# Kernel tuning notes

Hardware: AMD Instinct MI355X
Metric: run time of the kernel (lower is better)

## Reference

```python
import math
import jax, jax.numpy as jnp
import numpy as np

N_DIM = 1024
N_HEADS = 16
HEAD_DIM = N_DIM // N_HEADS
B, S = 8, 1024


def setup_inputs() -> dict:
    key = jax.random.key(0)
    ks = jax.random.split(key, 10)
    s = 1.0 / math.sqrt(N_DIM)
    inp = {
        "x": jax.random.normal(ks[0], (B, S, N_DIM), dtype=jnp.float32),
        "padding_mask": jax.random.randint(ks[1], (B, 1, 1, S), 0, 2).astype(bool),
        "Wq": jax.random.uniform(ks[2], (N_DIM, N_DIM), jnp.float32, -s, s),
        "bq": jax.random.uniform(ks[3], (N_DIM,), jnp.float32, -s, s),
        "Wk": jax.random.uniform(ks[4], (N_DIM, N_DIM), jnp.float32, -s, s),
        "bk": jax.random.uniform(ks[5], (N_DIM,), jnp.float32, -s, s),
        "Wv": jax.random.uniform(ks[6], (N_DIM, N_DIM), jnp.float32, -s, s),
        "bv": jax.random.uniform(ks[7], (N_DIM,), jnp.float32, -s, s),
        "Wo": jax.random.uniform(ks[8], (N_DIM, N_DIM), jnp.float32, -s, s),
        "bo": jax.random.uniform(ks[9], (N_DIM,), jnp.float32, -s, s),
    }
    return inp


def _split_heads(t):
    b, s, _ = t.shape
    return t.reshape(b, s, N_HEADS, HEAD_DIM).transpose(0, 2, 1, 3)  # [B,H,S,D]


def reference(x, padding_mask, Wq, bq, Wk, bk, Wv, bv, Wo, bo):
    # nn.Linear: y = x @ W^T + b
    Q = _split_heads(x @ Wq.T + bq)
    K = _split_heads(x @ Wk.T + bk)
    V = _split_heads(x @ Wv.T + bv)
    scale = 1.0 / math.sqrt(HEAD_DIM)
    scores = jnp.einsum('bhqd,bhkd->bhqk', Q, K) * scale
    scores = jnp.where(padding_mask, -jnp.inf, scores)
    attn = jax.nn.softmax(scores, axis=-1)
    attn = jnp.nan_to_num(attn, nan=0.0)  # fully-masked rows -> 0
    ctx = jnp.einsum('bhqk,bhkd->bhqd', attn, V)
    ctx = ctx.transpose(0, 2, 1, 3).reshape(x.shape[0], x.shape[1], N_DIM)
    return ctx @ Wo.T + bo  # dropout is identity in eval mode
```

## Files before the change

### kernel.cpp

```cpp
#include <hip/hip_runtime.h>
#include <hip/hip_bf16.h>
#include <math.h>

#define B_SZ 8
#define SEQ 1024
#define NDIM 1024
#define NH 16
#define HD 64
#define MROWS (B_SZ * SEQ)
#define SCALE_L2E 0.18033688011112042f
#define NEGB (-1e30f)

typedef __attribute__((ext_vector_type(4))) float f32x4;
typedef __attribute__((ext_vector_type(8))) short s16x8;
typedef __attribute__((ext_vector_type(4))) short s16x4;

#define MFMA16(a, b, c) __builtin_amdgcn_mfma_f32_16x16x32_bf16((a), (b), (c), 0, 0, 0)

__device__ __forceinline__ unsigned short f2bf(float f) {
    union { float f; unsigned int u; } v; v.f = f;
    unsigned int r = v.u + 0x7FFFu + ((v.u >> 16) & 1u);
    return (unsigned short)(r >> 16);
}

__device__ __forceinline__ void llds16(const void* g, void* l) {
    __builtin_amdgcn_global_load_lds(
        (const __attribute__((address_space(1))) void*)g,
        (__attribute__((address_space(3))) void*)l, 16, 0, 0);
}

__global__ void prep_mask(const unsigned char* __restrict__ m, float* __restrict__ bias) {
    __shared__ int fl[3];
    if (threadIdx.x < 3) fl[threadIdx.x] = 0;
    __syncthreads();
    int a = 0, o1 = 0, o23 = 0;
    for (int i = threadIdx.x; i < B_SZ * SEQ; i += 1024) {
        unsigned char v = m[i];
        if (v) { int q = i & 3; if (q == 0) a = 1; else if (q == 1) o1 = 1; else o23 = 1; }
    }
    if (a)   atomicOr(&fl[0], 1);
    if (o1)  atomicOr(&fl[1], 1);
    if (o23) atomicOr(&fl[2], 1);
    __syncthreads();
    int fmt;
    if (fl[0] && !fl[1] && !fl[2])      fmt = 0;
    else if (!fl[0] && !fl[1] && fl[2]) fmt = 2;
    else                                fmt = 1;
    for (int i = threadIdx.x; i < B_SZ * SEQ; i += 1024) {
        int t;
        if (fmt == 0)      t = ((const int*)m)[i];
        else if (fmt == 1) t = m[i];
        else               t = (((const float*)m)[i] != 0.f);
        bias[i] = t ? NEGB : 0.f;
    }
}

__global__ void cvt_x(const float* __restrict__ s, unsigned short* __restrict__ d) {
    const int i = (blockIdx.x * 256 + threadIdx.x) * 4;
    float4 v = *(const float4*)(s + i);
    s16x4 o; o[0] = (short)f2bf(v.x); o[1] = (short)f2bf(v.y);
    o[2] = (short)f2bf(v.z); o[3] = (short)f2bf(v.w);
    *(s16x4*)(d + i) = o;
}

__global__ void cvt_w(const float* __restrict__ q, const float* __restrict__ k,
                      const float* __restrict__ v, const float* __restrict__ o,
                      unsigned short* __restrict__ d) {
    const int i = (blockIdx.x * 256 + threadIdx.x) * 4;
    const int which = i >> 20;
    const float* s = (which == 0) ? q : (which == 1) ? k : (which == 2) ? v : o;
    float4 x = *(const float4*)(s + (i & ((1 << 20) - 1)));
    s16x4 p; p[0] = (short)f2bf(x.x); p[1] = (short)f2bf(x.y);
    p[2] = (short)f2bf(x.z); p[3] = (short)f2bf(x.w);
    *(s16x4*)(d + i) = p;
}

#define GBM 128
#define GBK 32

__global__ __launch_bounds__(256) void gemm_qkv(
    const unsigned short* __restrict__ X, const unsigned short* __restrict__ Wb,
    const float* __restrict__ bq, const float* __restrict__ bk, const float* __restrict__ bv,
    unsigned short* __restrict__ Qo, unsigned short* __restrict__ Ko,
    unsigned short* __restrict__ Vt)
{
    __shared__ __align__(16) short As[GBM * GBK];
    __shared__ __align__(16) short Bs[GBM * GBK];

    const int tid = threadIdx.x, lane = tid & 63, w = tid >> 6;
    const int wm = w >> 1, wn = w & 1;
    const int g = lane >> 4, ql = lane & 15;
    const int which = blockIdx.y >> 3, ny = blockIdx.y & 7;
    const int bm = blockIdx.x * GBM, bn = ny * GBM;
    const unsigned short* W = Wb + (size_t)which * (1 << 20);
    const float* bias = (which == 0) ? bq : (which == 1) ? bk : bv;

    f32x4 acc[4][4] = {};

    for (int k0 = 0; k0 < NDIM; k0 += GBK) {
#pragma unroll
        for (int i = 0; i < 2; ++i) {
            const int s = tid + i * 256;
            const int r = s >> 2, kc = (s & 3) * 8;
            llds16(X + (size_t)(bm + r) * NDIM + k0 + kc, &As[s * 8]);
            llds16(W + (size_t)(bn + r) * NDIM + k0 + kc, &Bs[s * 8]);
        }
        __syncthreads();
        s16x8 af[4], bf[4];
#pragma unroll
        for (int f = 0; f < 4; ++f) {
            af[f] = *(const s16x8*)&As[(wm * 64 + f * 16 + ql) * GBK + g * 8];
            bf[f] = *(const s16x8*)&Bs[(wn * 64 + f * 16 + ql) * GBK + g * 8];
        }
#pragma unroll
        for (int i = 0; i < 4; ++i)
#pragma unroll
            for (int j = 0; j < 4; ++j)
                acc[i][j] = MFMA16(af[i], bf[j], acc[i][j]);
        __syncthreads();
    }

    if (which < 2) {
        unsigned short* O = (which == 0) ? Qo : Ko;
#pragma unroll
        for (int j = 0; j < 4; ++j) {
            const int col = bn + wn * 64 + j * 16 + ql;
            const float bv_ = bias[col];
#pragma unroll
            for (int i = 0; i < 4; ++i) {
                const int row0 = bm + wm * 64 + i * 16 + 4 * g;
#pragma unroll
                for (int r = 0; r < 4; ++r)
                    O[(size_t)(row0 + r) * NDIM + col] = f2bf(acc[i][j][r] + bv_);
            }
        }
    } else {
#pragma unroll
        for (int j = 0; j < 4; ++j) {
            const int col = bn + wn * 64 + j * 16 + ql;
            const float bv_ = bias[col];
            const int h = col >> 6, dd = col & 63;
#pragma unroll
            for (int i = 0; i < 4; ++i) {
                const int row0 = bm + wm * 64 + i * 16 + 4 * g;
                const int b_ = row0 >> 10, s_ = row0 & 1023;
                s16x4 pk;
#pragma unroll
                for (int r = 0; r < 4; ++r) pk[r] = (short)f2bf(acc[i][j][r] + bv_);
                *(s16x4*)&Vt[(((size_t)(b_ * NH + h)) * HD + dd) * SEQ + s_] = pk;
            }
        }
    }
}

__global__ __launch_bounds__(256) void gemm_out(
    const unsigned short* __restrict__ X, const unsigned short* __restrict__ W,
    const float* __restrict__ bias, float* __restrict__ out)
{
    __shared__ __align__(16) short As[GBM * GBK];
    __shared__ __align__(16) short Bs[GBM * GBK];

    const int tid = threadIdx.x, lane = tid & 63, w = tid >> 6;
    const int wm = w >> 1, wn = w & 1;
    const int g = lane >> 4, ql = lane & 15;
    const int bm = blockIdx.x * GBM, bn = blockIdx.y * GBM;

    f32x4 acc[4][4] = {};

    for (int k0 = 0; k0 < NDIM; k0 += GBK) {
#pragma unroll
        for (int i = 0; i < 2; ++i) {
            const int s = tid + i * 256;
            const int r = s >> 2, kc = (s & 3) * 8;
            llds16(X + (size_t)(bm + r) * NDIM + k0 + kc, &As[s * 8]);
            llds16(W + (size_t)(bn + r) * NDIM + k0 + kc, &Bs[s * 8]);
        }
        __syncthreads();
        s16x8 af[4], bf[4];
#pragma unroll
        for (int f = 0; f < 4; ++f) {
            af[f] = *(const s16x8*)&As[(wm * 64 + f * 16 + ql) * GBK + g * 8];
            bf[f] = *(const s16x8*)&Bs[(wn * 64 + f * 16 + ql) * GBK + g * 8];
        }
#pragma unroll
        for (int i = 0; i < 4; ++i)
#pragma unroll
            for (int j = 0; j < 4; ++j)
                acc[i][j] = MFMA16(af[i], bf[j], acc[i][j]);
        __syncthreads();
    }

#pragma unroll
    for (int j = 0; j < 4; ++j) {
        const int col = bn + wn * 64 + j * 16 + ql;
        const float bv_ = bias[col];
#pragma unroll
        for (int i = 0; i < 4; ++i) {
            const int row0 = bm + wm * 64 + i * 16 + 4 * g;
#pragma unroll
            for (int r = 0; r < 4; ++r)
                out[(size_t)(row0 + r) * NDIM + col] = acc[i][j][r] + bv_;
        }
    }
}

__global__ __launch_bounds__(256) void attn(
    const unsigned short* __restrict__ Q, const unsigned short* __restrict__ K,
    const unsigned short* __restrict__ Vt, const float* __restrict__ maskB,
    unsigned short* __restrict__ ctx)
{
    __shared__ __align__(16) short Ks[64 * 64];
    __shared__ __align__(16) short Vs[80 * 64];
    __shared__ __align__(16) short Ps[4][16 * 72];

    const int tid = threadIdx.x, lane = tid & 63, w = tid >> 6;
    const int g = lane >> 4, ql = lane & 15;
    const int bh = blockIdx.x, b = bh >> 4, h = bh & 15;
    const int q0 = blockIdx.y * 64;

    {
        const int r = 64 + (tid >> 4), c = (tid & 15) * 4;
        const short v = (r == 64) ? (short)0x3F80 : (short)0;
        s16x4 pk = {v, v, v, v};
        *(s16x4*)&Vs[r * 64 + c] = pk;
    }

    const size_t qrow = (size_t)(b * SEQ + q0 + w * 16 + ql) * NDIM + h * HD;
    const s16x8 qa0 = *(const s16x8*)&Q[qrow + g * 8];
    const s16x8 qa1 = *(const s16x8*)&Q[qrow + 32 + g * 8];

    f32x4 o[5] = {};

    const unsigned short* Kb = K + (size_t)(b * SEQ) * NDIM + h * HD;
    const unsigned short* Vb = Vt + (size_t)bh * HD * SEQ;
    const float* mb = maskB + b * SEQ;
    short* Pp = &Ps[w][0];

    for (int kt = 0; kt < SEQ / 64; ++kt) {
        const int kv0 = kt * 64;
        s16x8 kr[2], vr[2];
#pragma unroll
        for (int i = 0; i < 2; ++i) {
            const int s = tid + i * 256;
            const int r = s >> 3, c8 = s & 7;
            kr[i] = *(const s16x8*)&Kb[(size_t)(kv0 + r) * NDIM + c8 * 8];
            vr[i] = *(const s16x8*)&Vb[(size_t)r * SEQ + kv0 + c8 * 8];
        }
        __syncthreads();
#pragma unroll
        for (int i = 0; i < 2; ++i) {
            const int s = tid + i * 256;
            const int r = s >> 3, c8 = s & 7;
            *(s16x8*)&Ks[r * 64 + ((c8 ^ (r & 7)) * 8)] = kr[i];
            *(s16x8*)&Vs[r * 64 + ((c8 ^ (r & 7)) * 8)] = vr[i];
        }
        __syncthreads();

        f32x4 sa[4] = {};
#pragma unroll
        for (int nt = 0; nt < 4; ++nt) {
            const int row = nt * 16 + ql;
            const s16x8 kb0 = *(const s16x8*)&Ks[row * 64 + (((g)     ^ (row & 7)) * 8)];
            const s16x8 kb1 = *(const s16x8*)&Ks[row * 64 + (((4 + g) ^ (row & 7)) * 8)];
            sa[nt] = MFMA16(qa0, kb0, sa[nt]);
            sa[nt] = MFMA16(qa1, kb1, sa[nt]);
        }

#pragma unroll
        for (int nt = 0; nt < 4; ++nt) {
            const float mbv = mb[kv0 + nt * 16 + ql];
#pragma unroll
            for (int r = 0; r < 4; ++r) {
                const float p = exp2f(fmaf(sa[nt][r], SCALE_L2E, mbv));
                Pp[(4 * g + r) * 72 + nt * 16 + ql] = (short)f2bf(p);
            }
        }
        const s16x8 pa0 = *(const s16x8*)&Pp[ql * 72 + 8 * g];
        const s16x8 pa1 = *(const s16x8*)&Pp[ql * 72 + 32 + 8 * g];

#pragma unroll
        for (int dt = 0; dt < 5; ++dt) {
            const int row = dt * 16 + ql;
            const s16x8 vb0 = *(const s16x8*)&Vs[row * 64 + (((g)     ^ (row & 7)) * 8)];
            const s16x8 vb1 = *(const s16x8*)&Vs[row * 64 + (((4 + g) ^ (row & 7)) * 8)];
            o[dt] = MFMA16(pa0, vb0, o[dt]);
            o[dt] = MFMA16(pa1, vb1, o[dt]);
        }
    }

    const int lsrc = lane & 48;
#pragma unroll
    for (int r = 0; r < 4; ++r) {
        const float lval = __shfl(o[4][r], lsrc);
        const float inv = (lval > 0.f) ? 1.f / lval : 0.f;
        const size_t row = (size_t)(b * SEQ + q0 + w * 16 + 4 * g + r) * NDIM + h * HD;
#pragma unroll
        for (int dt = 0; dt < 4; ++dt)
            ctx[row + dt * 16 + ql] = f2bf(o[dt][r] * inv);
    }
}

extern "C" void kernel_launch(void* const* d_in, const int* in_sizes, int n_in,
                              void* d_out, int out_size, void* d_ws, size_t ws_size,
                              hipStream_t stream)
{
    (void)in_sizes; (void)n_in; (void)out_size; (void)ws_size;
    const float* x  = (const float*)d_in[0];
    const unsigned char* mask = (const unsigned char*)d_in[1];
    const float* Wq = (const float*)d_in[2];
    const float* bq = (const float*)d_in[3];
    const float* Wk = (const float*)d_in[4];
    const float* bk = (const float*)d_in[5];
    const float* Wv = (const float*)d_in[6];
    const float* bv = (const float*)d_in[7];
    const float* Wo = (const float*)d_in[8];
    const float* bo = (const float*)d_in[9];
    float* out = (float*)d_out;

    char* ws = (char*)d_ws;
    float*          maskB = (float*)ws;
    unsigned short* xbf   = (unsigned short*)(ws + (32 << 10));
    unsigned short* wbf   = xbf + (size_t)MROWS * NDIM;
    unsigned short* Qbf   = wbf + (size_t)4 * NDIM * NDIM;
    unsigned short* Kbf   = Qbf + (size_t)MROWS * NDIM;
    unsigned short* Vtb   = Kbf + (size_t)MROWS * NDIM;
    unsigned short* Cbf   = Vtb + (size_t)MROWS * NDIM;

    prep_mask<<<1, 1024, 0, stream>>>(mask, maskB);
    cvt_x<<<MROWS * NDIM / 1024, 256, 0, stream>>>(x, xbf);
    cvt_w<<<4 * NDIM * NDIM / 1024, 256, 0, stream>>>(Wq, Wk, Wv, Wo, wbf);

    gemm_qkv<<<dim3(MROWS / GBM, 24), 256, 0, stream>>>(xbf, wbf, bq, bk, bv,
                                                        Qbf, Kbf, Vtb);
    attn<<<dim3(B_SZ * NH, SEQ / 64), 256, 0, stream>>>(Qbf, Kbf, Vtb, maskB, Cbf);
    gemm_out<<<dim3(MROWS / GBM, NDIM / GBM), 256, 0, stream>>>(
        Cbf, wbf + (size_t)3 * NDIM * NDIM, bo, out);
}
```

Baseline: 290.4 us.

## Widen GEMM K-tile with swizzled LDS, double attention KV block, merge convert kernels

GEMM kernels now stage 64-wide K tiles through a shared gemm_core with XOR-swizzled LDS layout, halving the number of barriers per K loop and reducing bank conflicts. The attention kernel processes 128 keys per iteration instead of 64, and the P matrix is rounded to bf16 by truncation instead of round-to-nearest. The x and weight conversion kernels are merged into one launch. These changes cut barrier, launch and rounding overhead but add LDS use and registers, which may lower occupancy, and truncation slightly changes numerics.

```diff
diff --git a/kernel.cpp b/kernel.cpp
--- a/kernel.cpp
+++ b/kernel.cpp
@@ -21,6 +21,10 @@
     union { float f; unsigned int u; } v; v.f = f;
     unsigned int r = v.u + 0x7FFFu + ((v.u >> 16) & 1u);
     return (unsigned short)(r >> 16);
+}
+__device__ __forceinline__ unsigned short f2bf_t(float f) {
+    union { float f; unsigned int u; } v; v.f = f;
+    return (unsigned short)(v.u >> 16);
 }
 
 __device__ __forceinline__ void llds16(const void* g, void* l) {
@@ -55,28 +59,71 @@
     }
 }
 
-__global__ void cvt_x(const float* __restrict__ s, unsigned short* __restrict__ d) {
-    const int i = (blockIdx.x * 256 + threadIdx.x) * 4;
-    float4 v = *(const float4*)(s + i);
-    s16x4 o; o[0] = (short)f2bf(v.x); o[1] = (short)f2bf(v.y);
-    o[2] = (short)f2bf(v.z); o[3] = (short)f2bf(v.w);
-    *(s16x4*)(d + i) = o;
-}
-
-__global__ void cvt_w(const float* __restrict__ q, const float* __restrict__ k,
-                      const float* __restrict__ v, const float* __restrict__ o,
-                      unsigned short* __restrict__ d) {
-    const int i = (blockIdx.x * 256 + threadIdx.x) * 4;
-    const int which = i >> 20;
-    const float* s = (which == 0) ? q : (which == 1) ? k : (which == 2) ? v : o;
-    float4 x = *(const float4*)(s + (i & ((1 << 20) - 1)));
-    s16x4 p; p[0] = (short)f2bf(x.x); p[1] = (short)f2bf(x.y);
-    p[2] = (short)f2bf(x.z); p[3] = (short)f2bf(x.w);
-    *(s16x4*)(d + i) = p;
+__global__ void cvt_all(const float* __restrict__ x,
+                        const float* __restrict__ wq, const float* __restrict__ wk,
+                        const float* __restrict__ wv, const float* __restrict__ wo,
+                        unsigned short* __restrict__ xbf, unsigned short* __restrict__ wbf)
+{
+    const int bid = blockIdx.x;
+    if (bid < MROWS * NDIM / 1024) {
+        const int i = bid * 1024 + threadIdx.x * 4;
+        float4 v = *(const float4*)(x + i);
+        s16x4 o; o[0] = (short)f2bf(v.x); o[1] = (short)f2bf(v.y);
+        o[2] = (short)f2bf(v.z); o[3] = (short)f2bf(v.w);
+        *(s16x4*)(xbf + i) = o;
+    } else {
+        const int j = (bid - MROWS * NDIM / 1024) * 1024 + threadIdx.x * 4;
+        const int which = j >> 20;
+        const float* s = (which == 0) ? wq : (which == 1) ? wk : (which == 2) ? wv : wo;
+        float4 v = *(const float4*)(s + (j & ((1 << 20) - 1)));
+        s16x4 o; o[0] = (short)f2bf(v.x); o[1] = (short)f2bf(v.y);
+        o[2] = (short)f2bf(v.z); o[3] = (short)f2bf(v.w);
+        *(s16x4*)(wbf + j) = o;
+    }
 }
 
 #define GBM 128
-#define GBK 32
+#define GBK 64
+
+#define STAGE_TILE(lds, src)                                              \
+    {                                                                     \
+_Pragma("unroll")                                                         \
+        for (int i = 0; i < 4; ++i) {                                     \
+            const int s = tid + i * 256;                                  \
+            const int r = s >> 3, c = s & 7;                              \
+            llds16((src) + (size_t)r * NDIM + ((c ^ (r & 7)) * 8),        \
+                   &(lds)[s * 8]);                                        \
+        }                                                                 \
+    }
+
+__device__ __forceinline__ void gemm_core(
+    const unsigned short* __restrict__ Xp, const unsigned short* __restrict__ Wp,
+    short* As, short* Bs, int tid, int wm, int wn, int g, int ql,
+    f32x4 acc[4][4])
+{
+    for (int k0 = 0; k0 < NDIM; k0 += GBK) {
+        STAGE_TILE(As, Xp + k0)
+        STAGE_TILE(Bs, Wp + k0)
+        __syncthreads();
+#pragma unroll
+        for (int kk = 0; kk < 2; ++kk) {
+            s16x8 af[4], bf[4];
+#pragma unroll
+            for (int f = 0; f < 4; ++f) {
+                const int ra = wm * 64 + f * 16 + ql;
+                const int rb = wn * 64 + f * 16 + ql;
+                af[f] = *(const s16x8*)&As[ra * 64 + (((kk * 4 + g) ^ (ra & 7)) * 8)];
+                bf[f] = *(const s16x8*)&Bs[rb * 64 + (((kk * 4 + g) ^ (rb & 7)) * 8)];
+            }
+#pragma unroll
+            for (int i = 0; i < 4; ++i)
+#pragma unroll
+                for (int j = 0; j < 4; ++j)
+                    acc[i][j] = MFMA16(af[i], bf[j], acc[i][j]);
+        }
+        __syncthreads();
+    }
+}
 
 __global__ __launch_bounds__(256) void gemm_qkv(
     const unsigned short* __restrict__ X, const unsigned short* __restrict__ Wb,
@@ -96,29 +143,8 @@
     const float* bias = (which == 0) ? bq : (which == 1) ? bk : bv;
 
     f32x4 acc[4][4] = {};
-
-    for (int k0 = 0; k0 < NDIM; k0 += GBK) {
-#pragma unroll
-        for (int i = 0; i < 2; ++i) {
-            const int s = tid + i * 256;
-            const int r = s >> 2, kc = (s & 3) * 8;
-            llds16(X + (size_t)(bm + r) * NDIM + k0 + kc, &As[s * 8]);
-            llds16(W + (size_t)(bn + r) * NDIM + k0 + kc, &Bs[s * 8]);
-        }
-        __syncthreads();
-        s16x8 af[4], bf[4];
-#pragma unroll
-        for (int f = 0; f < 4; ++f) {
-            af[f] = *(const s16x8*)&As[(wm * 64 + f * 16 + ql) * GBK + g * 8];
-            bf[f] = *(const s16x8*)&Bs[(wn * 64 + f * 16 + ql) * GBK + g * 8];
-        }
-#pragma unroll
-        for (int i = 0; i < 4; ++i)
-#pragma unroll
-            for (int j = 0; j < 4; ++j)
-                acc[i][j] = MFMA16(af[i], bf[j], acc[i][j]);
-        __syncthreads();
-    }
+    gemm_core(X + (size_t)bm * NDIM, W + (size_t)bn * NDIM,
+              As, Bs, tid, wm, wn, g, ql, acc);
 
     if (which < 2) {
         unsigned short* O = (which == 0) ? Qo : Ko;
@@ -166,29 +192,8 @@
     const int bm = blockIdx.x * GBM, bn = blockIdx.y * GBM;
 
     f32x4 acc[4][4] = {};
-
-    for (int k0 = 0; k0 < NDIM; k0 += GBK) {
-#pragma unroll
-        for (int i = 0; i < 2; ++i) {
-            const int s = tid + i * 256;
-            const int r = s >> 2, kc = (s & 3) * 8;
-            llds16(X + (size_t)(bm + r) * NDIM + k0 + kc, &As[s * 8]);
-            llds16(W + (size_t)(bn + r) * NDIM + k0 + kc, &Bs[s * 8]);
-        }
-        __syncthreads();
-        s16x8 af[4], bf[4];
-#pragma unroll
-        for (int f = 0; f < 4; ++f) {
-            af[f] = *(const s16x8*)&As[(wm * 64 + f * 16 + ql) * GBK + g * 8];
-            bf[f] = *(const s16x8*)&Bs[(wn * 64 + f * 16 + ql) * GBK + g * 8];
-        }
-#pragma unroll
-        for (int i = 0; i < 4; ++i)
-#pragma unroll
-            for (int j = 0; j < 4; ++j)
-                acc[i][j] = MFMA16(af[i], bf[j], acc[i][j]);
-        __syncthreads();
-    }
+    gemm_core(X + (size_t)bm * NDIM, W + (size_t)bn * NDIM,
+              As, Bs, tid, wm, wn, g, ql, acc);
 
 #pragma unroll
     for (int j = 0; j < 4; ++j) {
@@ -203,14 +208,16 @@
         }
     }
 }
+
+#define KVB 128
 
 __global__ __launch_bounds__(256) void attn(
     const unsigned short* __restrict__ Q, const unsigned short* __restrict__ K,
     const unsigned short* __restrict__ Vt, const float* __restrict__ maskB,
     unsigned short* __restrict__ ctx)
 {
-    __shared__ __align__(16) short Ks[64 * 64];
-    __shared__ __align__(16) short Vs[80 * 64];
+    __shared__ __align__(16) short Ks[KVB * 64];
+    __shared__ __align__(16) short Vs[80 * KVB];
     __shared__ __align__(16) short Ps[4][16 * 72];
 
     const int tid = threadIdx.x, lane = tid & 63, w = tid >> 6;
@@ -219,10 +226,10 @@
     const int q0 = blockIdx.y * 64;
 
     {
-        const int r = 64 + (tid >> 4), c = (tid & 15) * 4;
+        const int r = 64 + (tid >> 4), c = (tid & 15) * 8;
         const short v = (r == 64) ? (short)0x3F80 : (short)0;
-        s16x4 pk = {v, v, v, v};
-        *(s16x4*)&Vs[r * 64 + c] = pk;
+        s16x8 pk = {v, v, v, v, v, v, v, v};
+        *(s16x8*)&Vs[r * KVB + c] = pk;
     }
 
     const size_t qrow = (size_t)(b * SEQ + q0 + w * 16 + ql) * NDIM + h * HD;
@@ -236,29 +243,31 @@
     const float* mb = maskB + b * SEQ;
     short* Pp = &Ps[w][0];
 
-    for (int kt = 0; kt < SEQ / 64; ++kt) {
-        const int kv0 = kt * 64;
-        s16x8 kr[2], vr[2];
-#pragma unroll
-        for (int i = 0; i < 2; ++i) {
+    for (int kt = 0; kt < SEQ / KVB; ++kt) {
+        const int kv0 = kt * KVB;
+        s16x8 kr[4], vr[4];
+#pragma unroll
+        for (int i = 0; i < 4; ++i) {
             const int s = tid + i * 256;
-            const int r = s >> 3, c8 = s & 7;
-            kr[i] = *(const s16x8*)&Kb[(size_t)(kv0 + r) * NDIM + c8 * 8];
-            vr[i] = *(const s16x8*)&Vb[(size_t)r * SEQ + kv0 + c8 * 8];
+            const int rk = s >> 3, ck = s & 7;
+            const int rv = s >> 4, cv = s & 15;
+            kr[i] = *(const s16x8*)&Kb[(size_t)(kv0 + rk) * NDIM + ck * 8];
+            vr[i] = *(const s16x8*)&Vb[(size_t)rv * SEQ + kv0 + cv * 8];
         }
         __syncthreads();
 #pragma unroll
-        for (int i = 0; i < 2; ++i) {
+        for (int i = 0; i < 4; ++i) {
             const int s = tid + i * 256;
-            const int r = s >> 3, c8 = s & 7;
-            *(s16x8*)&Ks[r * 64 + ((c8 ^ (r & 7)) * 8)] = kr[i];
-            *(s16x8*)&Vs[r * 64 + ((c8 ^ (r & 7)) * 8)] = vr[i];
+            const int rk = s >> 3, ck = s & 7;
+            const int rv = s >> 4, cv = s & 15;
+            *(s16x8*)&Ks[rk * 64 + ((ck ^ (rk & 7)) * 8)] = kr[i];
+            *(s16x8*)&Vs[rv * KVB + ((cv ^ (rv & 7)) * 8)] = vr[i];
         }
         __syncthreads();
 
-        f32x4 sa[4] = {};
-#pragma unroll
-        for (int nt = 0; nt < 4; ++nt) {
+        f32x4 sa[8] = {};
+#pragma unroll
+        for (int nt = 0; nt < 8; ++nt) {
             const int row = nt * 16 + ql;
             const s16x8 kb0 = *(const s16x8*)&Ks[row * 64 + (((g)     ^ (row & 7)) * 8)];
             const s16x8 kb1 = *(const s16x8*)&Ks[row * 64 + (((4 + g) ^ (row & 7)) * 8)];
@@ -267,24 +276,27 @@
         }
 
 #pragma unroll
-        for (int nt = 0; nt < 4; ++nt) {
-            const float mbv = mb[kv0 + nt * 16 + ql];
-#pragma unroll
-            for (int r = 0; r < 4; ++r) {
-                const float p = exp2f(fmaf(sa[nt][r], SCALE_L2E, mbv));
-                Pp[(4 * g + r) * 72 + nt * 16 + ql] = (short)f2bf(p);
-            }
-        }
-        const s16x8 pa0 = *(const s16x8*)&Pp[ql * 72 + 8 * g];
-        const s16x8 pa1 = *(const s16x8*)&Pp[ql * 72 + 32 + 8 * g];
-
-#pragma unroll
-        for (int dt = 0; dt < 5; ++dt) {
-            const int row = dt * 16 + ql;
-            const s16x8 vb0 = *(const s16x8*)&Vs[row * 64 + (((g)     ^ (row & 7)) * 8)];
-            const s16x8 vb1 = *(const s16x8*)&Vs[row * 64 + (((4 + g) ^ (row & 7)) * 8)];
-            o[dt] = MFMA16(pa0, vb0, o[dt]);
-            o[dt] = MFMA16(pa1, vb1, o[dt]);
+        for (int h2 = 0; h2 < 2; ++h2) {
+#pragma unroll
+            for (int n4 = 0; n4 < 4; ++n4) {
+                const int nt = h2 * 4 + n4;
+                const float mbv = mb[kv0 + nt * 16 + ql];
+#pragma unroll
+                for (int r = 0; r < 4; ++r) {
+                    const float p = exp2f(fmaf(sa[nt][r], SCALE_L2E, mbv));
+                    Pp[(4 * g + r) * 72 + n4 * 16 + ql] = (short)f2bf_t(p);
+                }
+            }
+            const s16x8 pa0 = *(const s16x8*)&Pp[ql * 72 + 8 * g];
+            const s16x8 pa1 = *(const s16x8*)&Pp[ql * 72 + 32 + 8 * g];
+#pragma unroll
+            for (int dt = 0; dt < 5; ++dt) {
+                const int row = dt * 16 + ql;
+                const s16x8 vb0 = *(const s16x8*)&Vs[row * KVB + (((h2 * 8 + g)     ^ (row & 7)) * 8)];
+                const s16x8 vb1 = *(const s16x8*)&Vs[row * KVB + (((h2 * 8 + 4 + g) ^ (row & 7)) * 8)];
+                o[dt] = MFMA16(pa0, vb0, o[dt]);
+                o[dt] = MFMA16(pa1, vb1, o[dt]);
+            }
         }
     }
 
@@ -327,8 +339,8 @@
     unsigned short* Cbf   = Vtb + (size_t)MROWS * NDIM;
 
     prep_mask<<<1, 1024, 0, stream>>>(mask, maskB);
-    cvt_x<<<MROWS * NDIM / 1024, 256, 0, stream>>>(x, xbf);
-    cvt_w<<<4 * NDIM * NDIM / 1024, 256, 0, stream>>>(Wq, Wk, Wv, Wo, wbf);
+    cvt_all<<<(MROWS * NDIM + 4 * NDIM * NDIM) / 1024, 256, 0, stream>>>(
+        x, Wq, Wk, Wv, Wo, xbf, wbf);
 
     gemm_qkv<<<dim3(MROWS / GBM, 24), 256, 0, stream>>>(xbf, wbf, bq, bk, bv,
                                                         Qbf, Kbf, Vtb);
```

After: 287.8 us. About the same (-0.9%).
